# Kernel optimization log

Measured on AMD Instinct MI355X. Metric: run time of the kernel, lower is better.

Reference implementation:

```python
import jax, jax.numpy as jnp
import numpy as np

HEADS = 8
DIM_HEAD = 32
SCALE = DIM_HEAD ** -0.5
EPS = 1e-12  # F.normalize eps


def _rmsnorm_ch(t, g):
    # F.normalize(t, dim=1) * g * sqrt(C)  (normalize_dim=1)
    c = t.shape[1]
    norm = jnp.sqrt(jnp.sum(t * t, axis=1, keepdims=True))
    return t / jnp.maximum(norm, EPS) * g[None, :, None, None] * (c ** 0.5)


def setup_inputs() -> dict:
    key = jax.random.key(0)
    ks = jax.random.split(key, 4)
    B, C, H, W = 16, 256, 64, 64
    hidden = HEADS * DIM_HEAD  # 256
    x = jax.random.normal(ks[0], (B, C, H, W), dtype=jnp.float32)
    g1 = jnp.ones((C,), dtype=jnp.float32)
    # conv 1x1 weights stored as [out_ch, in_ch]
    w_qkv = jax.random.normal(ks[1], (hidden * 3, C), dtype=jnp.float32) * (1.0 / np.sqrt(C))
    w_out = jax.random.normal(ks[2], (C, hidden), dtype=jnp.float32) * (1.0 / np.sqrt(hidden))
    b_out = jnp.zeros((C,), dtype=jnp.float32)
    g2 = jnp.ones((C,), dtype=jnp.float32)
    return {"x": x, "g1": g1, "w_qkv": w_qkv, "w_out": w_out, "b_out": b_out, "g2": g2}


def reference(x, g1, w_qkv, w_out, b_out, g2):
    b, c, h, w = x.shape
    n = h * w
    xn = _rmsnorm_ch(x, g1)
    # 1x1 conv (no bias) == channel matmul
    qkv = jnp.einsum('oc,bchw->bohw', w_qkv, xn)
    q, k, v = jnp.split(qkv, 3, axis=1)
    # b (h c) x y -> b h c (x y)
    q = q.reshape(b, HEADS, DIM_HEAD, n)
    k = k.reshape(b, HEADS, DIM_HEAD, n)
    v = v.reshape(b, HEADS, DIM_HEAD, n)
    q = jax.nn.softmax(q, axis=-2) * SCALE  # softmax over dim_head
    k = jax.nn.softmax(k, axis=-1)          # softmax over sequence
    context = jnp.einsum('bhdn,bhen->bhde', k, v)  # [b,h,d,e] small
    out = jnp.einsum('bhde,bhdn->bhen', context, q)
    out = out.reshape(b, HEADS * DIM_HEAD, h, w)
    out = jnp.einsum('oc,bchw->bohw', w_out, out) + b_out[None, :, None, None]
    return _rmsnorm_ch(out, g2) + x
```

## Files before the change

kernel.cpp:

```cpp
#include <hip/hip_runtime.h>
#include <math.h>


#define B_ 16
#define C_ 256
#define N_ 4096
#define SCALE_ 0.17677669529663687f
#define EPS_ 1e-12f

typedef __attribute__((ext_vector_type(8))) short bf16x8;
typedef __attribute__((ext_vector_type(4))) float f32x4;

__device__ __forceinline__ ushort f2bf(float f) {
    union { float f; uint u; } x; x.f = f;
    uint r = (x.u + 0x7FFFu + ((x.u >> 16) & 1u)) >> 16;
    return (ushort)r;
}
__device__ __forceinline__ float bf2f(ushort s) {
    union { uint u; float f; } x; x.u = ((uint)s) << 16;
    return x.f;
}

__global__ __launch_bounds__(256) void k_prep(const float* __restrict__ w_qkv,
                                              const float* __restrict__ g1,
                                              ushort* __restrict__ Wp) {
    int o = blockIdx.x, c = threadIdx.x;
    Wp[(size_t)o * 256 + c] = f2bf(w_qkv[(size_t)o * 256 + c] * g1[c]);
}

__global__ __launch_bounds__(256) void k_xconv(const float* __restrict__ x,
                                               ushort* __restrict__ xnbT) {
    __shared__ float ssp[4][64];
    __shared__ float rinv_s[64];
    __shared__ ushort T[64][268];
    int b = blockIdx.y, n0 = blockIdx.x * 64;
    const float* xb = x + (size_t)b * C_ * N_ + n0;
    int t = threadIdx.x;
    int nl = t & 63, cg = t >> 6;
    float ss = 0.f;
    #pragma unroll 8
    for (int i = 0; i < 64; ++i) {
        float v = xb[(size_t)(cg * 64 + i) * N_ + nl];
        ss += v * v;
    }
    ssp[cg][nl] = ss;
    __syncthreads();
    if (t < 64)
        rinv_s[t] = 16.f / fmaxf(sqrtf(ssp[0][t] + ssp[1][t] + ssp[2][t] + ssp[3][t]), EPS_);
    __syncthreads();
    float rv = rinv_s[nl];
    #pragma unroll 8
    for (int i = 0; i < 64; ++i) {
        int c = cg * 64 + i;
        T[nl][c] = f2bf(xb[(size_t)c * N_ + nl] * rv);
    }
    __syncthreads();
    int j = t >> 2, ch = t & 3;
    ushort* orow = xnbT + ((size_t)b * N_ + n0 + j) * 256 + ch * 64;
    #pragma unroll
    for (int i = 0; i < 8; ++i)
        *(uint2*)&orow[i * 8] = *(const uint2*)&T[j][ch * 64 + i * 8],
        *(uint2*)&orow[i * 8 + 4] = *(const uint2*)&T[j][ch * 64 + i * 8 + 4];
}

__global__ __launch_bounds__(512) void k_kvctx(const ushort* __restrict__ Wp,
                                               const ushort* __restrict__ xnbT,
                                               float* __restrict__ ctxp,
                                               float* __restrict__ sums_p) {
    extern __shared__ char lds[];
    ushort (*Asub)[40] = (ushort(*)[40])lds;
    char* BQ = lds + 20480;
    char* P  = lds + 86016;
    const int b = blockIdx.y, s = blockIdx.x;
    const int col0 = s * 128;
    const int t = threadIdx.x, l = t & 63, w = t >> 6;
    const int lr = l & 15, grp = l >> 4;
    const int wn = w & 3, wo = w >> 2;
    const ushort* xb = xnbT + (size_t)b * N_ * 256;

    {
        int row = t >> 2, seg = t & 3;
        const uint4* src = (const uint4*)(xb + (size_t)(col0 + row) * 256 + seg * 64);
        uint base = (uint)(row * 512 + seg * 128);
        uint sw = (uint)((row & 7) << 4);
        #pragma unroll
        for (int i = 0; i < 8; ++i)
            *(uint4*)(BQ + ((base + i * 16) ^ sw)) = src[i];
    }

    #pragma unroll
    for (int p = 0; p < 2; ++p) {
        f32x4 acc[2][8] = {};
        for (int k0 = 0; k0 < 256; k0 += 32) {
            {
                int r = t >> 1, ko = (t & 1) * 16;
                const uint4* sa = (const uint4*)(Wp + (size_t)(256 + p * 256 + r) * 256 + k0 + ko);
                *(uint4*)&Asub[r][ko]     = sa[0];
                *(uint4*)&Asub[r][ko + 8] = sa[1];
            }
            __syncthreads();
            bf16x8 ax[2], bw[8];
            #pragma unroll
            for (int m = 0; m < 2; ++m) {
                int row = wn * 32 + m * 16 + lr;
                uint off = (uint)(row * 512 + (k0 + grp * 8) * 2) ^ (uint)((row & 7) << 4);
                ax[m] = *(const bf16x8*)(BQ + off);
            }
            #pragma unroll
            for (int nf = 0; nf < 8; ++nf)
                bw[nf] = *(const bf16x8*)&Asub[wo * 128 + nf * 16 + lr][grp * 8];
            #pragma unroll
            for (int m = 0; m < 2; ++m)
                #pragma unroll
                for (int nf = 0; nf < 8; ++nf)
                    acc[m][nf] = __builtin_amdgcn_mfma_f32_16x16x32_bf16(ax[m], bw[nf], acc[m][nf], 0, 0, 0);
            __syncthreads();
        }
        if (p == 0) {
            #pragma unroll
            for (int nf = 0; nf < 8; ++nf) {
                int d = wo * 128 + nf * 16 + lr;
                uint sw = (uint)((d & 7) << 4);
                #pragma unroll
                for (int m = 0; m < 2; ++m) {
                    int n0 = wn * 32 + m * 16 + grp * 4;
                    uint2 pk;
                    pk.x = (uint)f2bf(__expf(acc[m][nf][0])) | ((uint)f2bf(__expf(acc[m][nf][1])) << 16);
                    pk.y = (uint)f2bf(__expf(acc[m][nf][2])) | ((uint)f2bf(__expf(acc[m][nf][3])) << 16);
                    *(uint2*)(P + (((uint)(d * 256 + n0 * 2)) ^ sw)) = pk;
                }
            }
        } else {
            #pragma unroll
            for (int nf = 0; nf < 8; ++nf) {
                int e = wo * 128 + nf * 16 + lr;
                uint sw = (uint)((e & 7) << 4);
                #pragma unroll
                for (int m = 0; m < 2; ++m) {
                    int n0 = wn * 32 + m * 16 + grp * 4;
                    uint2 pk;
                    pk.x = (uint)f2bf(acc[m][nf][0]) | ((uint)f2bf(acc[m][nf][1]) << 16);
                    pk.y = (uint)f2bf(acc[m][nf][2]) | ((uint)f2bf(acc[m][nf][3]) << 16);
                    *(uint2*)(BQ + (((uint)(e * 256 + n0 * 2)) ^ sw)) = pk;
                }
            }
        }
    }
    __syncthreads();

    const int h = w;
    f32x4 c3[2][2] = {};
    f32x4 cS[2] = {};
    bf16x8 ones;
    #pragma unroll
    for (int j = 0; j < 8; ++j) ones[j] = (short)0x3F80;
    #pragma unroll
    for (int ks = 0; ks < 4; ++ks) {
        int n0 = ks * 32 + grp * 8;
        bf16x8 pA[2], vB[2];
        #pragma unroll
        for (int df = 0; df < 2; ++df) {
            int d = h * 32 + df * 16 + lr;
            pA[df] = *(const bf16x8*)(P + (((uint)(d * 256 + n0 * 2)) ^ ((uint)((d & 7) << 4))));
        }
        #pragma unroll
        for (int ef = 0; ef < 2; ++ef) {
            int e = h * 32 + ef * 16 + lr;
            vB[ef] = *(const bf16x8*)(BQ + (((uint)(e * 256 + n0 * 2)) ^ ((uint)((e & 7) << 4))));
        }
        #pragma unroll
        for (int df = 0; df < 2; ++df) {
            #pragma unroll
            for (int ef = 0; ef < 2; ++ef)
                c3[df][ef] = __builtin_amdgcn_mfma_f32_16x16x32_bf16(pA[df], vB[ef], c3[df][ef], 0, 0, 0);
            cS[df] = __builtin_amdgcn_mfma_f32_16x16x32_bf16(pA[df], ones, cS[df], 0, 0, 0);
        }
    }
    int bh = b * 8 + h;
    size_t base = ((size_t)s * 128 + bh) * 32;
    #pragma unroll
    for (int df = 0; df < 2; ++df) {
        #pragma unroll
        for (int ef = 0; ef < 2; ++ef)
            #pragma unroll
            for (int r = 0; r < 4; ++r)
                ctxp[(base + df * 16 + grp * 4 + r) * 32 + ef * 16 + lr] = c3[df][ef][r];
        if (lr == 0)
            #pragma unroll
            for (int r = 0; r < 4; ++r)
                sums_p[base + df * 16 + grp * 4 + r] = cS[df][r];
    }
}

__global__ __launch_bounds__(256) void k_fold(const float* __restrict__ w_out,
                                              const float* __restrict__ ctxp,
                                              const float* __restrict__ sums_p,
                                              ushort* __restrict__ M) {
    __shared__ float cn[32][33];
    __shared__ float sinv[32];
    int bh = blockIdx.x;
    int b = bh >> 3, h = bh & 7;
    int t = threadIdx.x;
    if (t < 32) {
        float st = 0.f;
        #pragma unroll 8
        for (int s = 0; s < 32; ++s) st += sums_p[(size_t)(s * 128 + bh) * 32 + t];
        sinv[t] = SCALE_ / st;
    }
    #pragma unroll
    for (int i = t; i < 1024; i += 256) {
        int d = i >> 5, e = i & 31;
        float cv = 0.f;
        #pragma unroll 8
        for (int s = 0; s < 32; ++s)
            cv += ctxp[((size_t)(s * 128 + bh) * 32 + d) * 32 + e];
        cn[e][d] = cv;
    }
    __syncthreads();
    float wreg[32];
    const float* wr = w_out + (size_t)t * 256 + h * 32;
    #pragma unroll
    for (int e = 0; e < 32; e += 4) {
        float4 wv = *(const float4*)&wr[e];
        wreg[e] = wv.x; wreg[e + 1] = wv.y; wreg[e + 2] = wv.z; wreg[e + 3] = wv.w;
    }
    float acc[32] = {};
    #pragma unroll
    for (int e = 0; e < 32; ++e) {
        float we = wreg[e];
        #pragma unroll
        for (int d = 0; d < 32; ++d) acc[d] += we * cn[e][d];
    }
    ushort* Mrow = M + ((size_t)b * 256 + t) * 256 + h * 32;
    #pragma unroll
    for (int d = 0; d < 32; ++d) Mrow[d] = f2bf(acc[d] * sinv[d]);
}

__global__ __launch_bounds__(512) void k_qfinal(const ushort* __restrict__ Wp,
                                                const ushort* __restrict__ xnbT,
                                                const ushort* __restrict__ M,
                                                const float* __restrict__ b_out,
                                                const float* __restrict__ g2,
                                                const float* __restrict__ x,
                                                float* __restrict__ out) {
    __shared__ ushort BQ[64 * 256];
    __shared__ float ss2[8][64];
    const int b = blockIdx.y, col0 = blockIdx.x * 64;
    const int t = threadIdx.x, l = t & 63, w = t >> 6;
    const int lr = l & 15, grp = l >> 4;
    const ushort* xb = xnbT + (size_t)b * N_ * 256;

    {
        int row = t >> 3, seg = t & 7;
        const uint4* src = (const uint4*)(xb + (size_t)(col0 + row) * 256 + seg * 32);
        uint base = (uint)(row * 512 + seg * 64);
        uint sw = (uint)((row & 7) << 4);
        #pragma unroll
        for (int i = 0; i < 4; ++i)
            *(uint4*)((char*)BQ + ((base + i * 16) ^ sw)) = src[i];
    }
    __syncthreads();

    f32x4 acc[2][4] = {};
    for (int k0 = 0; k0 < 256; k0 += 32) {
        bf16x8 af[2], bf[4];
        #pragma unroll
        for (int m = 0; m < 2; ++m)
            af[m] = *(const bf16x8*)(Wp + (size_t)(w * 32 + m * 16 + lr) * 256 + k0 + grp * 8);
        #pragma unroll
        for (int n = 0; n < 4; ++n) {
            int row = n * 16 + lr;
            uint off = (uint)(row * 512 + (k0 + grp * 8) * 2) ^ (uint)((row & 7) << 4);
            bf[n] = *(const bf16x8*)((const char*)BQ + off);
        }
        #pragma unroll
        for (int m = 0; m < 2; ++m)
            #pragma unroll
            for (int n = 0; n < 4; ++n)
                acc[m][n] = __builtin_amdgcn_mfma_f32_16x16x32_bf16(af[m], bf[n], acc[m][n], 0, 0, 0);
    }
    __syncthreads();

    #pragma unroll
    for (int n = 0; n < 4; ++n) {
        float f[2][4];
        #pragma unroll
        for (int m = 0; m < 2; ++m)
            #pragma unroll
            for (int r = 0; r < 4; ++r) f[m][r] = acc[m][n][r];
        float mx = -1e30f;
        #pragma unroll
        for (int r = 0; r < 4; ++r) mx = fmaxf(mx, fmaxf(f[0][r], f[1][r]));
        mx = fmaxf(mx, __shfl_xor(mx, 16));
        mx = fmaxf(mx, __shfl_xor(mx, 32));
        float s = 0.f;
        #pragma unroll
        for (int r = 0; r < 4; ++r) {
            f[0][r] = __expf(f[0][r] - mx); s += f[0][r];
            f[1][r] = __expf(f[1][r] - mx); s += f[1][r];
        }
        s += __shfl_xor(s, 16); s += __shfl_xor(s, 32);
        float inv = 1.f / s;
        int cl = n * 16 + lr;
        #pragma unroll
        for (int m = 0; m < 2; ++m) {
            int d = w * 32 + m * 16 + grp * 4;
            uint2 pk;
            pk.x = (uint)f2bf(f[m][0] * inv) | ((uint)f2bf(f[m][1] * inv) << 16);
            pk.y = (uint)f2bf(f[m][2] * inv) | ((uint)f2bf(f[m][3] * inv) << 16);
            uint off = (uint)(cl * 512 + d * 2) ^ (uint)((cl & 7) << 4);
            *(uint2*)((char*)BQ + off) = pk;
        }
    }
    __syncthreads();

    f32x4 acc2[2][4] = {};
    const ushort* Mb = M + (size_t)b * 256 * 256;
    for (int k0 = 0; k0 < 256; k0 += 32) {
        bf16x8 af[2], bq[4];
        #pragma unroll
        for (int m = 0; m < 2; ++m)
            af[m] = *(const bf16x8*)(Mb + (size_t)(w * 32 + m * 16 + lr) * 256 + k0 + grp * 8);
        #pragma unroll
        for (int n = 0; n < 4; ++n) {
            int row = n * 16 + lr;
            uint off = (uint)(row * 512 + (k0 + grp * 8) * 2) ^ (uint)((row & 7) << 4);
            bq[n] = *(const bf16x8*)((const char*)BQ + off);
        }
        #pragma unroll
        for (int m = 0; m < 2; ++m)
            #pragma unroll
            for (int n = 0; n < 4; ++n)
                acc2[m][n] = __builtin_amdgcn_mfma_f32_16x16x32_bf16(af[m], bq[n], acc2[m][n], 0, 0, 0);
    }

    #pragma unroll
    for (int n = 0; n < 4; ++n) {
        float local = 0.f;
        #pragma unroll
        for (int m = 0; m < 2; ++m) {
            int obase = w * 32 + m * 16 + grp * 4;
            #pragma unroll
            for (int r = 0; r < 4; ++r) {
                float f = acc2[m][n][r] + b_out[obase + r];
                acc2[m][n][r] = f;
                local += f * f;
            }
        }
        local += __shfl_xor(local, 16);
        local += __shfl_xor(local, 32);
        if (grp == 0) ss2[w][n * 16 + lr] = local;
    }
    __syncthreads();
    const float* xb2 = x + (size_t)b * C_ * N_;
    float* ob = out + (size_t)b * C_ * N_;
    #pragma unroll
    for (int n = 0; n < 4; ++n) {
        int cl = n * 16 + lr;
        int cg = col0 + cl;
        float tot = ss2[0][cl] + ss2[1][cl] + ss2[2][cl] + ss2[3][cl]
                  + ss2[4][cl] + ss2[5][cl] + ss2[6][cl] + ss2[7][cl];
        float rs = 16.f / fmaxf(sqrtf(tot), EPS_);
        #pragma unroll
        for (int m = 0; m < 2; ++m) {
            int obase = w * 32 + m * 16 + grp * 4;
            #pragma unroll
            for (int r = 0; r < 4; ++r) {
                int o = obase + r;
                ob[(size_t)o * N_ + cg] = acc2[m][n][r] * rs * g2[o] + xb2[(size_t)o * N_ + cg];
            }
        }
    }
}

extern "C" void kernel_launch(void* const* d_in, const int* in_sizes, int n_in,
                              void* d_out, int out_size, void* d_ws, size_t ws_size,
                              hipStream_t stream) {
    const float* x     = (const float*)d_in[0];
    const float* g1    = (const float*)d_in[1];
    const float* w_qkv = (const float*)d_in[2];
    const float* w_out = (const float*)d_in[3];
    const float* b_out = (const float*)d_in[4];
    const float* g2    = (const float*)d_in[5];
    float* out = (float*)d_out;
    char* ws = (char*)d_ws;

    ushort* Wp     = (ushort*)(ws + 0);
    float*  ctxp   = (float*)(ws + 393216);
    float*  sums_p = (float*)(ws + 17170432);
    ushort* Mm     = (ushort*)(ws + 17694720);
    ushort* xnbT   = (ushort*)(ws + 19791872);

    hipFuncSetAttribute((const void*)k_kvctx,
                        hipFuncAttributeMaxDynamicSharedMemorySize, 151552);

    k_prep<<<768, 256, 0, stream>>>(w_qkv, g1, Wp);
    k_xconv<<<dim3(64, 16), 256, 0, stream>>>(x, xnbT);
    k_kvctx<<<dim3(32, 16), 512, 151552, stream>>>(Wp, xnbT, ctxp, sums_p);
    k_fold<<<128, 256, 0, stream>>>(w_out, ctxp, sums_p, Mm);
    k_qfinal<<<dim3(64, 16), 512, 0, stream>>>(Wp, xnbT, Mm, b_out, g2, x, out);
}
```

Baseline: 146.5 us.

## Fuse input RMS-norm and bf16 transpose into kvctx and qfinal kernels

Removes the separate k_xconv kernel that normalized x and wrote a transposed bf16 copy to workspace. Instead, k_kvctx and k_qfinal each read fp32 x directly, compute per-column sum of squares, scale, convert to bf16 and write the swizzled LDS tile themselves. This drops one launch and the round-trip of the 32 MB bf16 intermediate. In exchange x is read twice per consumer (once for the norm, once for conversion), and the fp32 reads are strided column loads. A barrier is added before ss2 is reused in k_qfinal.

After: 134.2 us. -8.4%, faster.

```diff
diff --git a/kernel.cpp b/kernel.cpp
--- a/kernel.cpp
+++ b/kernel.cpp
@@ -28,64 +28,51 @@
     Wp[(size_t)o * 256 + c] = f2bf(w_qkv[(size_t)o * 256 + c] * g1[c]);
 }
 
-__global__ __launch_bounds__(256) void k_xconv(const float* __restrict__ x,
-                                               ushort* __restrict__ xnbT) {
-    __shared__ float ssp[4][64];
-    __shared__ float rinv_s[64];
-    __shared__ ushort T[64][268];
-    int b = blockIdx.y, n0 = blockIdx.x * 64;
-    const float* xb = x + (size_t)b * C_ * N_ + n0;
-    int t = threadIdx.x;
-    int nl = t & 63, cg = t >> 6;
-    float ss = 0.f;
-    #pragma unroll 8
-    for (int i = 0; i < 64; ++i) {
-        float v = xb[(size_t)(cg * 64 + i) * N_ + nl];
-        ss += v * v;
-    }
-    ssp[cg][nl] = ss;
-    __syncthreads();
-    if (t < 64)
-        rinv_s[t] = 16.f / fmaxf(sqrtf(ssp[0][t] + ssp[1][t] + ssp[2][t] + ssp[3][t]), EPS_);
-    __syncthreads();
-    float rv = rinv_s[nl];
-    #pragma unroll 8
-    for (int i = 0; i < 64; ++i) {
-        int c = cg * 64 + i;
-        T[nl][c] = f2bf(xb[(size_t)c * N_ + nl] * rv);
-    }
-    __syncthreads();
-    int j = t >> 2, ch = t & 3;
-    ushort* orow = xnbT + ((size_t)b * N_ + n0 + j) * 256 + ch * 64;
-    #pragma unroll
-    for (int i = 0; i < 8; ++i)
-        *(uint2*)&orow[i * 8] = *(const uint2*)&T[j][ch * 64 + i * 8],
-        *(uint2*)&orow[i * 8 + 4] = *(const uint2*)&T[j][ch * 64 + i * 8 + 4];
-}
-
 __global__ __launch_bounds__(512) void k_kvctx(const ushort* __restrict__ Wp,
-                                               const ushort* __restrict__ xnbT,
+                                               const float* __restrict__ x,
                                                float* __restrict__ ctxp,
                                                float* __restrict__ sums_p) {
     extern __shared__ char lds[];
     ushort (*Asub)[40] = (ushort(*)[40])lds;
     char* BQ = lds + 20480;
     char* P  = lds + 86016;
+    float* sspA  = (float*)(lds + 151552);
+    float* rinvA = (float*)(lds + 153600);
     const int b = blockIdx.y, s = blockIdx.x;
     const int col0 = s * 128;
     const int t = threadIdx.x, l = t & 63, w = t >> 6;
     const int lr = l & 15, grp = l >> 4;
     const int wn = w & 3, wo = w >> 2;
-    const ushort* xb = xnbT + (size_t)b * N_ * 256;
+    const float* xb = x + (size_t)b * C_ * N_ + col0;
 
     {
-        int row = t >> 2, seg = t & 3;
-        const uint4* src = (const uint4*)(xb + (size_t)(col0 + row) * 256 + seg * 64);
-        uint base = (uint)(row * 512 + seg * 128);
-        uint sw = (uint)((row & 7) << 4);
-        #pragma unroll
-        for (int i = 0; i < 8; ++i)
-            *(uint4*)(BQ + ((base + i * 16) ^ sw)) = src[i];
+        int col = t & 127, rg = t >> 7;
+        float ss = 0.f;
+        #pragma unroll 8
+        for (int i = 0; i < 64; ++i) {
+            float v = xb[(size_t)(rg * 64 + i) * N_ + col];
+            ss += v * v;
+        }
+        sspA[rg * 128 + col] = ss;
+    }
+    __syncthreads();
+    if (t < 128)
+        rinvA[t] = 16.f / fmaxf(sqrtf(sspA[t] + sspA[128 + t] + sspA[256 + t] + sspA[384 + t]), EPS_);
+    __syncthreads();
+    {
+        int col = t & 127, rg = t >> 7;
+        float rv = rinvA[col];
+        uint sw = (uint)((col & 7) << 4);
+        #pragma unroll
+        for (int i = 0; i < 16; ++i) {
+            int c = rg * 64 + i * 4;
+            uint2 pk;
+            pk.x = (uint)f2bf(xb[(size_t)c * N_ + col] * rv)
+                 | ((uint)f2bf(xb[(size_t)(c + 1) * N_ + col] * rv) << 16);
+            pk.y = (uint)f2bf(xb[(size_t)(c + 2) * N_ + col] * rv)
+                 | ((uint)f2bf(xb[(size_t)(c + 3) * N_ + col] * rv) << 16);
+            *(uint2*)(BQ + (((uint)(col * 512 + c * 2)) ^ sw)) = pk;
+        }
     }
 
     #pragma unroll
@@ -237,7 +224,6 @@
 }
 
 __global__ __launch_bounds__(512) void k_qfinal(const ushort* __restrict__ Wp,
-                                                const ushort* __restrict__ xnbT,
                                                 const ushort* __restrict__ M,
                                                 const float* __restrict__ b_out,
                                                 const float* __restrict__ g2,
@@ -245,19 +231,43 @@
                                                 float* __restrict__ out) {
     __shared__ ushort BQ[64 * 256];
     __shared__ float ss2[8][64];
+    __shared__ float rinvq[64];
     const int b = blockIdx.y, col0 = blockIdx.x * 64;
     const int t = threadIdx.x, l = t & 63, w = t >> 6;
     const int lr = l & 15, grp = l >> 4;
-    const ushort* xb = xnbT + (size_t)b * N_ * 256;
+    const float* xb2 = x + (size_t)b * C_ * N_;
 
     {
-        int row = t >> 3, seg = t & 7;
-        const uint4* src = (const uint4*)(xb + (size_t)(col0 + row) * 256 + seg * 32);
-        uint base = (uint)(row * 512 + seg * 64);
-        uint sw = (uint)((row & 7) << 4);
-        #pragma unroll
-        for (int i = 0; i < 4; ++i)
-            *(uint4*)((char*)BQ + ((base + i * 16) ^ sw)) = src[i];
+        int col = t & 63, rg = t >> 6;
+        float ss = 0.f;
+        #pragma unroll 8
+        for (int i = 0; i < 32; ++i) {
+            float v = xb2[(size_t)(rg * 32 + i) * N_ + col0 + col];
+            ss += v * v;
+        }
+        ss2[rg][col] = ss;
+    }
+    __syncthreads();
+    if (t < 64) {
+        float st = ss2[0][t] + ss2[1][t] + ss2[2][t] + ss2[3][t]
+                 + ss2[4][t] + ss2[5][t] + ss2[6][t] + ss2[7][t];
+        rinvq[t] = 16.f / fmaxf(sqrtf(st), EPS_);
+    }
+    __syncthreads();
+    {
+        int col = t & 63, rg = t >> 6;
+        float rv = rinvq[col];
+        uint sw = (uint)((col & 7) << 4);
+        #pragma unroll
+        for (int i = 0; i < 8; ++i) {
+            int c = rg * 32 + i * 4;
+            uint2 pk;
+            pk.x = (uint)f2bf(xb2[(size_t)c * N_ + col0 + col] * rv)
+                 | ((uint)f2bf(xb2[(size_t)(c + 1) * N_ + col0 + col] * rv) << 16);
+            pk.y = (uint)f2bf(xb2[(size_t)(c + 2) * N_ + col0 + col] * rv)
+                 | ((uint)f2bf(xb2[(size_t)(c + 3) * N_ + col0 + col] * rv) << 16);
+            *(uint2*)((char*)BQ + (((uint)(col * 512 + c * 2)) ^ sw)) = pk;
+        }
     }
     __syncthreads();
 
@@ -334,6 +344,7 @@
                 acc2[m][n] = __builtin_amdgcn_mfma_f32_16x16x32_bf16(af[m], bq[n], acc2[m][n], 0, 0, 0);
     }
 
+    __syncthreads();
     #pragma unroll
     for (int n = 0; n < 4; ++n) {
         float local = 0.f;
@@ -352,7 +363,6 @@
         if (grp == 0) ss2[w][n * 16 + lr] = local;
     }
     __syncthreads();
-    const float* xb2 = x + (size_t)b * C_ * N_;
     float* ob = out + (size_t)b * C_ * N_;
     #pragma unroll
     for (int n = 0; n < 4; ++n) {
@@ -389,14 +399,12 @@
     float*  ctxp   = (float*)(ws + 393216);
     float*  sums_p = (float*)(ws + 17170432);
     ushort* Mm     = (ushort*)(ws + 17694720);
-    ushort* xnbT   = (ushort*)(ws + 19791872);
 
     hipFuncSetAttribute((const void*)k_kvctx,
-                        hipFuncAttributeMaxDynamicSharedMemorySize, 151552);
+                        hipFuncAttributeMaxDynamicSharedMemorySize, 154112);
 
     k_prep<<<768, 256, 0, stream>>>(w_qkv, g1, Wp);
-    k_xconv<<<dim3(64, 16), 256, 0, stream>>>(x, xnbT);
-    k_kvctx<<<dim3(32, 16), 512, 151552, stream>>>(Wp, xnbT, ctxp, sums_p);
+    k_kvctx<<<dim3(32, 16), 512, 154112, stream>>>(Wp, x, ctxp, sums_p);
     k_fold<<<128, 256, 0, stream>>>(w_out, ctxp, sums_p, Mm);
-    k_qfinal<<<dim3(64, 16), 512, 0, stream>>>(Wp, xnbT, Mm, b_out, g2, x, out);
-}
+    k_qfinal<<<dim3(64, 16), 512, 0, stream>>>(Wp, Mm, b_out, g2, x, out);
+}
```
